# Kernel optimization log

Hardware: AMD Instinct MI355X
Metric: run time of the kernel (lower is better)

The kernel has to match this reference:

```python
import jax, jax.numpy as jnp
import numpy as np
import math

B, Z, D = 1024, 32768, 128

def setup_inputs() -> dict:
    key = jax.random.key(0)
    k1, k2, k3 = jax.random.split(key, 3)
    z_sparse = jax.random.randint(k1, (B, Z), 0, 2, dtype=jnp.int32)
    context_embedding = jax.random.normal(k2, (B, D), dtype=jnp.float32)
    embd_table = jax.random.normal(k3, (Z, D), dtype=jnp.float32)  # nn.Embedding weight
    return {"z_sparse": z_sparse, "context_embedding": context_embedding, "embd_table": embd_table}

def reference(z_sparse, context_embedding, embd_table):
    # mask[b, z] = feature z active in batch b  (matches (z_sparse > 0).nonzero())
    mask = z_sparse > 0  # [B, Z]
    # attn_scores = (ctx * emb).sum(-1) / sqrt(D), densified over all (b, z)
    scores = (context_embedding @ embd_table.T) / math.sqrt(embd_table.shape[1])  # [B, Z]
    # per-batch softmax over active features only
    masked = jnp.where(mask, scores, -jnp.inf)
    w = jax.nn.softmax(masked, axis=-1)
    w = jnp.where(mask, w, 0.0)  # zero inactive (also kills NaN for all-empty rows)
    # scatter-add of emb * weight == weighted matmul against the table
    out = w @ embd_table  # [B, D]
    counts = jnp.clip(jnp.sum(mask, axis=-1), 1, None)  # bincount(...).clamp(min=1)
    return out / counts[:, None].astype(out.dtype)
```

## Files before the change

### kernel.cpp

```cpp
#include <hip/hip_runtime.h>
#include <stdint.h>

#define B_SZ 1024
#define Z_SZ 32768
#define D_SZ 128
#define NZ   32
#define CZ   (Z_SZ / NZ)
#define TZ   64
#define ITERS (CZ / TZ)
#define TBLK 64
#define WROWS 16
#define ZW   (Z_SZ / 32)

#define SEMB_STRIDE  136
#define SEMBT_STRIDE 72
#define SP_STRIDE    72
#define ST_STRIDE    136

#define NB_MASK ((B_SZ * ZW) / 256)
#define NB_TAB  (Z_SZ / 64)

#define WS_O   0
#define WS_M   (NZ * B_SZ * D_SZ)
#define WS_L   (WS_M + NZ * B_SZ)
#define WS_C   (WS_L + NZ * B_SZ)
#define WS_TAB (WS_C + NZ * B_SZ)

typedef short bf16x8 __attribute__((ext_vector_type(8)));
typedef float f32x4  __attribute__((ext_vector_type(4)));

#if __has_builtin(__builtin_amdgcn_exp2f)
#define EXP2F(x) __builtin_amdgcn_exp2f(x)
#else
#define EXP2F(x) exp2f(x)
#endif

__device__ __forceinline__ unsigned short f2bf(float f) {
    union { float f; uint32_t u; } v; v.f = f;
    uint32_t u = v.u;
    u = (u + 0x7FFFu + ((u >> 16) & 1u)) >> 16;
    return (unsigned short)u;
}

__global__ __launch_bounds__(256) void prep(
    const int*      __restrict__ zs,
    const float*    __restrict__ emb,
    unsigned short* __restrict__ embR,
    unsigned short* __restrict__ embT,
    uint32_t*       __restrict__ maskp)
{
    __shared__ __align__(16) unsigned short st[64 * ST_STRIDE];
    if (blockIdx.x < NB_MASK) {
        const int gid = blockIdx.x * 256 + threadIdx.x;
        const int4* src = (const int4*)(zs + (size_t)gid * 32);
        uint32_t mbits = 0;
#pragma unroll
        for (int k = 0; k < 8; ++k) {
            int4 v = src[k];
            mbits |= (v.x > 0 ? 1u : 0u) << (4 * k + 0);
            mbits |= (v.y > 0 ? 1u : 0u) << (4 * k + 1);
            mbits |= (v.z > 0 ? 1u : 0u) << (4 * k + 2);
            mbits |= (v.w > 0 ? 1u : 0u) << (4 * k + 3);
        }
        maskp[gid] = mbits;
        return;
    }

    const int z0 = (blockIdx.x - NB_MASK) * 64;
    const int t  = threadIdx.x;
    {
        const int r = t >> 2, q = t & 3;
        const float* src = emb + (size_t)(z0 + r) * D_SZ + q * 32;
        unsigned short* dR = embR + (size_t)(z0 + r) * D_SZ + q * 32;
        unsigned short* dL = st + r * ST_STRIDE + q * 32;
#pragma unroll
        for (int u = 0; u < 8; ++u) {
            float4 x = *(const float4*)(src + 4 * u);
            ushort4 h;
            h.x = f2bf(x.x); h.y = f2bf(x.y); h.z = f2bf(x.z); h.w = f2bf(x.w);
            *(ushort4*)(dR + 4 * u) = h;
            *(ushort4*)(dL + 4 * u) = h;
        }
    }
    __syncthreads();
    {
        const int lane = t & 63, w = t >> 6;
#pragma unroll
        for (int i = 0; i < 4; ++i) {
            const int d = w * 32 + i * 8 + (lane >> 3);
            const int c = lane & 7;
            bf16x8 v;
#pragma unroll
            for (int k = 0; k < 8; ++k) v[k] = (short)st[(c * 8 + k) * ST_STRIDE + d];
            *(bf16x8*)(embT + (size_t)d * Z_SZ + z0 + c * 8) = v;
        }
    }
}

__global__ __launch_bounds__(256, 2) void attn_part(
    const uint32_t*       __restrict__ maskp,
    const float*          __restrict__ ctx,
    const unsigned short* __restrict__ embR,
    const unsigned short* __restrict__ embT,
    float*                __restrict__ ws)
{
    __shared__ __align__(16) unsigned short s_emb [TZ   * SEMB_STRIDE];
    __shared__ __align__(16) unsigned short s_embT[D_SZ * SEMBT_STRIDE];
    __shared__ __align__(16) unsigned short s_P   [4 * WROWS * SP_STRIDE];

    const int tid  = threadIdx.x;
    const int wave = tid >> 6;
    const int lane = tid & 63;
    const int l15  = lane & 15;
    const int quad = lane >> 4;

    const int bg     = blockIdx.x;
    const int ch     = blockIdx.y;
    const int z_base = ch * CZ;
    const int wb0    = bg * TBLK + wave * WROWS;
    const int brow   = wb0 + l15;

    const int srow = tid >> 2, sq3 = tid & 3;
    const int sd   = tid >> 1, sh  = tid & 1;

    bf16x8 afrag[4];
    {
        const float scale = (float)(1.4426950408889634 * 0.08838834764831845);
        const float* crow = ctx + (size_t)brow * D_SZ;
#pragma unroll
        for (int ks = 0; ks < 4; ++ks) {
            const float* p = crow + ks * 32 + quad * 8;
            float4 x0 = *(const float4*)(p);
            float4 x1 = *(const float4*)(p + 4);
            bf16x8 a;
            a[0] = (short)f2bf(x0.x * scale); a[1] = (short)f2bf(x0.y * scale);
            a[2] = (short)f2bf(x0.z * scale); a[3] = (short)f2bf(x0.w * scale);
            a[4] = (short)f2bf(x1.x * scale); a[5] = (short)f2bf(x1.y * scale);
            a[6] = (short)f2bf(x1.z * scale); a[7] = (short)f2bf(x1.w * scale);
            afrag[ks] = a;
        }
    }

    float m_s = -1e30f, l_s = 0.f;
    int   cnt = 0;
    f32x4 acc2[8];
#pragma unroll
    for (int n = 0; n < 8; ++n) { acc2[n][0]=0.f; acc2[n][1]=0.f; acc2[n][2]=0.f; acc2[n][3]=0.f; }

    bf16x8 rA[4], rT[4];
    uint2  mv, mvn;
    {
        const unsigned short* srcR = embR + (size_t)(z_base + srow) * D_SZ + sq3 * 32;
        const unsigned short* srcT = embT + (size_t)sd * Z_SZ + z_base + sh * 32;
#pragma unroll
        for (int u = 0; u < 4; ++u) {
            rA[u] = *(const bf16x8*)(srcR + u * 8);
            rT[u] = *(const bf16x8*)(srcT + u * 8);
        }
        mv = *(const uint2*)(maskp + (size_t)brow * ZW + (z_base >> 5));
    }

    for (int it = 0; it < ITERS; ++it) {
        __syncthreads();

        {
            unsigned short* dst = s_emb + srow * SEMB_STRIDE + sq3 * 32;
#pragma unroll
            for (int u = 0; u < 4; ++u) *(bf16x8*)(dst + u * 8) = rA[u];
        }
        {
            unsigned short* dst = s_embT + sd * SEMBT_STRIDE + sh * 32;
#pragma unroll
            for (int u = 0; u < 4; ++u) *(bf16x8*)(dst + u * 8) = rT[u];
        }

        __syncthreads();

        if (it + 1 < ITERS) {
            const int z0n = z_base + (it + 1) * TZ;
            const unsigned short* srcR = embR + (size_t)(z0n + srow) * D_SZ + sq3 * 32;
            const unsigned short* srcT = embT + (size_t)sd * Z_SZ + z0n + sh * 32;
#pragma unroll
            for (int u = 0; u < 4; ++u) {
                rA[u] = *(const bf16x8*)(srcR + u * 8);
                rT[u] = *(const bf16x8*)(srcT + u * 8);
            }
            mvn = *(const uint2*)(maskp + (size_t)brow * ZW + (z0n >> 5));
        }

        f32x4 sfr[4];
#pragma unroll
        for (int nt = 0; nt < 4; ++nt) {
            f32x4 c; c[0]=0.f; c[1]=0.f; c[2]=0.f; c[3]=0.f;
            const unsigned short* bb = s_emb + (nt * 16 + l15) * SEMB_STRIDE + quad * 8;
#pragma unroll
            for (int ks = 0; ks < 4; ++ks) {
                bf16x8 ef = *(const bf16x8*)(bb + ks * 32);
                c = __builtin_amdgcn_mfma_f32_16x16x32_bf16(ef, afrag[ks], c, 0, 0, 0);
            }
            sfr[nt] = c;
        }

        const uint32_t w0 = mv.x >> (quad * 4);
        const uint32_t w1 = mv.y >> (quad * 4);
        int bit[4][4];
#pragma unroll
        for (int r = 0; r < 4; ++r) {
            bit[0][r] = (int)((w0 >> (r))      & 1u);
            bit[1][r] = (int)((w0 >> (16 + r)) & 1u);
            bit[2][r] = (int)((w1 >> (r))      & 1u);
            bit[3][r] = (int)((w1 >> (16 + r)) & 1u);
        }
        cnt += __popc(mv.x) + __popc(mv.y);

        float tm = -1e30f;
#pragma unroll
        for (int nt = 0; nt < 4; ++nt) {
            float a0 = bit[nt][0] ? sfr[nt][0] : -1e30f;
            float a1 = bit[nt][1] ? sfr[nt][1] : -1e30f;
            float a2 = bit[nt][2] ? sfr[nt][2] : -1e30f;
            float a3 = bit[nt][3] ? sfr[nt][3] : -1e30f;
            tm = fmaxf(tm, fmaxf(fmaxf(a0, a1), fmaxf(a2, a3)));
        }
        tm = fmaxf(tm, __shfl_xor(tm, 16));
        tm = fmaxf(tm, __shfl_xor(tm, 32));

        if (__any(tm > m_s + 8.f)) {
            float mnew = fmaxf(m_s, tm);
            float al = EXP2F(m_s - mnew);
            m_s = mnew;
            l_s *= al;
#pragma unroll
            for (int n = 0; n < 8; ++n) acc2[n] *= al;
        }

        unsigned short* pwv = s_P + wave * (WROWS * SP_STRIDE) + l15 * SP_STRIDE + quad * 4;
        float ps = 0.f;
#pragma unroll
        for (int nt = 0; nt < 4; ++nt) {
            float p0 = bit[nt][0] ? EXP2F(sfr[nt][0] - m_s) : 0.f;
            float p1 = bit[nt][1] ? EXP2F(sfr[nt][1] - m_s) : 0.f;
            float p2 = bit[nt][2] ? EXP2F(sfr[nt][2] - m_s) : 0.f;
            float p3 = bit[nt][3] ? EXP2F(sfr[nt][3] - m_s) : 0.f;
            ps += (p0 + p1) + (p2 + p3);
            ushort4 h;
            h.x = f2bf(p0); h.y = f2bf(p1); h.z = f2bf(p2); h.w = f2bf(p3);
            *(ushort4*)(pwv + nt * 16) = h;
        }
        ps += __shfl_xor(ps, 16);
        ps += __shfl_xor(ps, 32);
        l_s += ps;

        const unsigned short* pb = s_P + wave * (WROWS * SP_STRIDE) + l15 * SP_STRIDE + quad * 8;
        bf16x8 pA0 = *(const bf16x8*)(pb);
        bf16x8 pA1 = *(const bf16x8*)(pb + 32);
#pragma unroll
        for (int nt2 = 0; nt2 < 8; ++nt2) {
            const unsigned short* tb = s_embT + (nt2 * 16 + l15) * SEMBT_STRIDE + quad * 8;
            bf16x8 e0 = *(const bf16x8*)(tb);
            bf16x8 e1 = *(const bf16x8*)(tb + 32);
            acc2[nt2] = __builtin_amdgcn_mfma_f32_16x16x32_bf16(e0, pA0, acc2[nt2], 0, 0, 0);
            acc2[nt2] = __builtin_amdgcn_mfma_f32_16x16x32_bf16(e1, pA1, acc2[nt2], 0, 0, 0);
        }

        mv = mvn;
    }

    {
        float* orow = ws + WS_O + ((size_t)ch * B_SZ + brow) * D_SZ;
#pragma unroll
        for (int nt2 = 0; nt2 < 8; ++nt2) {
            *(f32x4*)(orow + nt2 * 16 + quad * 4) = acc2[nt2];
        }
    }
    if (lane < 16) {
        ws[WS_M + ch * B_SZ + brow] = m_s;
        ws[WS_L + ch * B_SZ + brow] = l_s;
        ws[WS_C + ch * B_SZ + brow] = (float)cnt;
    }
}

__global__ __launch_bounds__(128) void attn_reduce(
    const float* __restrict__ ws, float* __restrict__ out)
{
    const int b = blockIdx.x;
    const int d = threadIdx.x;
    const float* mP = ws + WS_M;
    const float* lP = ws + WS_L;
    const float* cP = ws + WS_C;

    float M = -1e30f;
#pragma unroll
    for (int c = 0; c < NZ; ++c) M = fmaxf(M, mP[c * B_SZ + b]);

    float L = 0.f, C = 0.f, acc = 0.f;
#pragma unroll
    for (int c = 0; c < NZ; ++c) {
        float w = EXP2F(mP[c * B_SZ + b] - M);
        L += lP[c * B_SZ + b] * w;
        C += cP[c * B_SZ + b];
        acc += ws[WS_O + ((size_t)c * B_SZ + b) * D_SZ + d] * w;
    }
    float cntv = fmaxf(C, 1.0f);
    out[(size_t)b * D_SZ + d] = (L > 0.f) ? acc / (L * cntv) : 0.f;
}

extern "C" void kernel_launch(void* const* d_in, const int* in_sizes, int n_in,
                              void* d_out, int out_size, void* d_ws, size_t ws_size,
                              hipStream_t stream) {
    (void)in_sizes; (void)n_in; (void)out_size; (void)ws_size;
    const int*   zs  = (const int*)  d_in[0];
    const float* ctx = (const float*)d_in[1];
    const float* emb = (const float*)d_in[2];
    float* out = (float*)d_out;
    float* ws  = (float*)d_ws;

    unsigned short* embR  = (unsigned short*)(ws + WS_TAB);
    unsigned short* embT  = embR + (size_t)Z_SZ * D_SZ;
    uint32_t*       maskp = (uint32_t*)(embT + (size_t)Z_SZ * D_SZ);

    prep<<<NB_MASK + NB_TAB, 256, 0, stream>>>(zs, emb, embR, embT, maskp);

    dim3 grid1(B_SZ / TBLK, NZ);
    attn_part<<<grid1, 256, 0, stream>>>(maskp, ctx, embR, embT, ws);
    attn_reduce<<<B_SZ, 128, 0, stream>>>(ws, out);
}
```

Measured before the change: 253.9 us.

## Fuse mask bit-packing into attention kernel by reading int32 mask directly

Drops the mask bit-packing blocks from the prep kernel. The attention kernel now loads the raw int32 z_sparse values for its rows as int4 vectors, double-buffered alongside the table tiles, and derives the active bits and per-row counts in registers. This removes a separate full pass over the large mask plus the packed mask write and read. In exchange, the main loop issues heavier, less coalesced global loads and holds more registers for prefetched mask values, which may hurt occupancy or latency hiding.

```diff
diff --git a/kernel.cpp b/kernel.cpp
--- a/kernel.cpp
+++ b/kernel.cpp
@@ -10,14 +10,12 @@
 #define ITERS (CZ / TZ)
 #define TBLK 64
 #define WROWS 16
-#define ZW   (Z_SZ / 32)
 
 #define SEMB_STRIDE  136
 #define SEMBT_STRIDE 72
 #define SP_STRIDE    72
 #define ST_STRIDE    136
 
-#define NB_MASK ((B_SZ * ZW) / 256)
 #define NB_TAB  (Z_SZ / 64)
 
 #define WS_O   0
@@ -43,30 +41,12 @@
 }
 
 __global__ __launch_bounds__(256) void prep(
-    const int*      __restrict__ zs,
     const float*    __restrict__ emb,
     unsigned short* __restrict__ embR,
-    unsigned short* __restrict__ embT,
-    uint32_t*       __restrict__ maskp)
+    unsigned short* __restrict__ embT)
 {
     __shared__ __align__(16) unsigned short st[64 * ST_STRIDE];
-    if (blockIdx.x < NB_MASK) {
-        const int gid = blockIdx.x * 256 + threadIdx.x;
-        const int4* src = (const int4*)(zs + (size_t)gid * 32);
-        uint32_t mbits = 0;
-#pragma unroll
-        for (int k = 0; k < 8; ++k) {
-            int4 v = src[k];
-            mbits |= (v.x > 0 ? 1u : 0u) << (4 * k + 0);
-            mbits |= (v.y > 0 ? 1u : 0u) << (4 * k + 1);
-            mbits |= (v.z > 0 ? 1u : 0u) << (4 * k + 2);
-            mbits |= (v.w > 0 ? 1u : 0u) << (4 * k + 3);
-        }
-        maskp[gid] = mbits;
-        return;
-    }
-
-    const int z0 = (blockIdx.x - NB_MASK) * 64;
+    const int z0 = blockIdx.x * 64;
     const int t  = threadIdx.x;
     {
         const int r = t >> 2, q = t & 3;
@@ -98,7 +78,7 @@
 }
 
 __global__ __launch_bounds__(256, 2) void attn_part(
-    const uint32_t*       __restrict__ maskp,
+    const int*            __restrict__ zs,
     const float*          __restrict__ ctx,
     const unsigned short* __restrict__ embR,
     const unsigned short* __restrict__ embT,
@@ -122,6 +102,8 @@
 
     const int srow = tid >> 2, sq3 = tid & 3;
     const int sd   = tid >> 1, sh  = tid & 1;
+
+    const int* zrow = zs + (size_t)brow * Z_SZ + quad * 4;
 
     bf16x8 afrag[4];
     {
@@ -148,7 +130,7 @@
     for (int n = 0; n < 8; ++n) { acc2[n][0]=0.f; acc2[n][1]=0.f; acc2[n][2]=0.f; acc2[n][3]=0.f; }
 
     bf16x8 rA[4], rT[4];
-    uint2  mv, mvn;
+    int4   mc[4], mn[4];
     {
         const unsigned short* srcR = embR + (size_t)(z_base + srow) * D_SZ + sq3 * 32;
         const unsigned short* srcT = embT + (size_t)sd * Z_SZ + z_base + sh * 32;
@@ -157,7 +139,8 @@
             rA[u] = *(const bf16x8*)(srcR + u * 8);
             rT[u] = *(const bf16x8*)(srcT + u * 8);
         }
-        mv = *(const uint2*)(maskp + (size_t)brow * ZW + (z_base >> 5));
+#pragma unroll
+        for (int nt = 0; nt < 4; ++nt) mc[nt] = *(const int4*)(zrow + z_base + nt * 16);
     }
 
     for (int it = 0; it < ITERS; ++it) {
@@ -185,7 +168,8 @@
                 rA[u] = *(const bf16x8*)(srcR + u * 8);
                 rT[u] = *(const bf16x8*)(srcT + u * 8);
             }
-            mvn = *(const uint2*)(maskp + (size_t)brow * ZW + (z0n >> 5));
+#pragma unroll
+            for (int nt = 0; nt < 4; ++nt) mn[nt] = *(const int4*)(zrow + z0n + nt * 16);
         }
 
         f32x4 sfr[4];
@@ -201,17 +185,15 @@
             sfr[nt] = c;
         }
 
-        const uint32_t w0 = mv.x >> (quad * 4);
-        const uint32_t w1 = mv.y >> (quad * 4);
         int bit[4][4];
 #pragma unroll
-        for (int r = 0; r < 4; ++r) {
-            bit[0][r] = (int)((w0 >> (r))      & 1u);
-            bit[1][r] = (int)((w0 >> (16 + r)) & 1u);
-            bit[2][r] = (int)((w1 >> (r))      & 1u);
-            bit[3][r] = (int)((w1 >> (16 + r)) & 1u);
-        }
-        cnt += __popc(mv.x) + __popc(mv.y);
+        for (int nt = 0; nt < 4; ++nt) {
+            bit[nt][0] = (mc[nt].x > 0) ? 1 : 0;
+            bit[nt][1] = (mc[nt].y > 0) ? 1 : 0;
+            bit[nt][2] = (mc[nt].z > 0) ? 1 : 0;
+            bit[nt][3] = (mc[nt].w > 0) ? 1 : 0;
+            cnt += bit[nt][0] + bit[nt][1] + bit[nt][2] + bit[nt][3];
+        }
 
         float tm = -1e30f;
 #pragma unroll
@@ -263,7 +245,8 @@
             acc2[nt2] = __builtin_amdgcn_mfma_f32_16x16x32_bf16(e1, pA1, acc2[nt2], 0, 0, 0);
         }
 
-        mv = mvn;
+#pragma unroll
+        for (int nt = 0; nt < 4; ++nt) mc[nt] = mn[nt];
     }
 
     {
@@ -273,6 +256,8 @@
             *(f32x4*)(orow + nt2 * 16 + quad * 4) = acc2[nt2];
         }
     }
+    cnt += __shfl_xor(cnt, 16);
+    cnt += __shfl_xor(cnt, 32);
     if (lane < 16) {
         ws[WS_M + ch * B_SZ + brow] = m_s;
         ws[WS_L + ch * B_SZ + brow] = l_s;
@@ -315,13 +300,12 @@
     float* out = (float*)d_out;
     float* ws  = (float*)d_ws;
 
-    unsigned short* embR  = (unsigned short*)(ws + WS_TAB);
-    unsigned short* embT  = embR + (size_t)Z_SZ * D_SZ;
-    uint32_t*       maskp = (uint32_t*)(embT + (size_t)Z_SZ * D_SZ);
-
-    prep<<<NB_MASK + NB_TAB, 256, 0, stream>>>(zs, emb, embR, embT, maskp);
+    unsigned short* embR = (unsigned short*)(ws + WS_TAB);
+    unsigned short* embT = embR + (size_t)Z_SZ * D_SZ;
+
+    prep<<<NB_TAB, 256, 0, stream>>>(emb, embR, embT);
 
     dim3 grid1(B_SZ / TBLK, NZ);
-    attn_part<<<grid1, 256, 0, stream>>>(maskp, ctx, embR, embT, ws);
+    attn_part<<<grid1, 256, 0, stream>>>(zs, ctx, embR, embT, ws);
     attn_reduce<<<B_SZ, 128, 0, stream>>>(ws, out);
 }
```

Result: faster. 240.6 us (-5.2%).
